# Performance work log

Hardware: AMD Instinct MI355X
Metric: run time of the kernel (lower is better)

Reference implementation:

```python
import jax, jax.numpy as jnp
import numpy as np

BATCH, T, C = 32, 600, 64
DEPTH = 2            # logsig depth 2 -> [increments, Levy areas]
N_SEGMENTS = 50
N_HIDDENS = 512
LOGSIG_CH = C + C * (C - 1) // 2   # 2080, Lyndon-word count at depth 2
IN_SIZE = C + LOGSIG_CH            # 2144 = logsig + start point


def _t_vec(nT, n_segments):
    # matches: [int(round(x)) for x in np.linspace(1, nT, n_segments+1)]
    return np.asarray([int(round(v)) for v in np.linspace(1, nT, n_segments + 1)])


def setup_inputs() -> dict:
    key = jax.random.key(0)
    k0, k1, k2, k3, k4 = jax.random.split(key, 5)
    x = jax.random.normal(k0, (BATCH, T, C), jnp.float32)
    s = 1.0 / np.sqrt(N_HIDDENS)
    w_ih = jax.random.uniform(k1, (4 * N_HIDDENS, IN_SIZE), jnp.float32, -s, s)
    w_hh = jax.random.uniform(k2, (4 * N_HIDDENS, N_HIDDENS), jnp.float32, -s, s)
    b_ih = jax.random.uniform(k3, (4 * N_HIDDENS,), jnp.float32, -s, s)
    b_hh = jax.random.uniform(k4, (4 * N_HIDDENS,), jnp.float32, -s, s)
    return {"x": x, "w_ih": w_ih, "w_hh": w_hh, "b_ih": b_ih, "b_hh": b_hh}


def _logsig_and_start(x):
    """Depth-2 segmented log-signature + segment start points.
    Returns (logsig (B,S,LOGSIG_CH), start (B,S,C))."""
    B, nT, c = x.shape
    tv = _t_vec(nT, N_SEGMENTS)
    starts = tv[:-1] - 1               # segment start frame indices
    ends = tv[1:] - 1                  # segment end frame indices
    # step s (between frames s and s+1) belongs to segment i iff tv[i]-1 <= s < tv[i+1]-1
    step_ids = jnp.asarray(np.searchsorted(tv[1:] - 1, np.arange(nT - 1), side='right'))
    dx = x[:, 1:] - x[:, :-1]                            # (B, T-1, C)
    # per-step outer product x_{t-} (X) dx_t, then segmented sum over steps
    prod = jnp.einsum('btc,btd->btcd', x[:, :-1], dx)    # (B, T-1, C, C)
    Q = jax.ops.segment_sum(jnp.moveaxis(prod, 1, 0), step_ids,
                            num_segments=N_SEGMENTS)      # (S, B, C, C)
    xa = x[:, starts]                                    # (B, S, C)
    xb = x[:, ends]
    inc = xb - xa                                        # level-1 logsig
    # shift origin to segment start: P = sum (X_rel (X) dX)
    P = jnp.moveaxis(Q, 0, 1) - jnp.einsum('bsc,bsd->bscd', xa, inc)
    A = 0.5 * (P - jnp.swapaxes(P, -1, -2))              # Levy area (antisym)
    iu, ju = np.triu_indices(c, 1)                       # Lyndon words (i,j), i<j, lex order
    logsig = jnp.concatenate([inc, A[:, :, iu, ju]], axis=-1)
    return logsig, xa


def _lstm(feats, w_ih, w_hh, b_ih, b_hh):
    B = feats.shape[0]
    H = N_HIDDENS
    gx = jnp.einsum('bsf,gf->bsg', feats, w_ih) + b_ih + b_hh  # (B,S,4H)

    def step(carry, g_t):
        h, cc = carry
        g = g_t + h @ w_hh.T
        i, f, gg, o = jnp.split(g, 4, axis=-1)
        i = jax.nn.sigmoid(i); f = jax.nn.sigmoid(f)
        gg = jnp.tanh(gg); o = jax.nn.sigmoid(o)
        cc = f * cc + i * gg
        h = o * jnp.tanh(cc)
        return (h, cc), h

    h0 = jnp.zeros((B, H), feats.dtype)
    (_, _), hs = jax.lax.scan(step, (h0, h0), jnp.moveaxis(gx, 1, 0))
    return jnp.moveaxis(hs, 0, 1)                        # (B, S, H)


def reference(x, w_ih, w_hh, b_ih, b_hh):
    logsig, x_sp = _logsig_and_start(x)
    feats = jnp.concatenate([logsig, x_sp], axis=-1)      # (B, S, IN_SIZE)
    return _lstm(feats, w_ih, w_hh, b_ih, b_hh)
```

## Files before the change

### kernel.cpp

```cpp
#include <hip/hip_runtime.h>
#include <math.h>

typedef _Float16 f16;
typedef _Float16 f16x8 __attribute__((ext_vector_type(8)));
typedef _Float16 f16x4 __attribute__((ext_vector_type(4)));
typedef float    f32x4 __attribute__((ext_vector_type(4)));

#define BATCH 32
#define TT    600
#define CC    64
#define SEG   50
#define HH    512
#define G4    2048
#define FF    2144
#define MM    1600
#define MP    1664
#define NPAIR 2016
#define CVB   512
#define WRK   208
#define SLOT16 16384

struct TV { int v[51]; };

__device__ __forceinline__ void async_copy16(char* lds, const char* g) {
  __builtin_amdgcn_global_load_lds(
      (const __attribute__((address_space(1))) unsigned int*)g,
      (__attribute__((address_space(3))) unsigned int*)lds, 16, 0, 0);
}

__device__ __forceinline__ float sigm(float x) { return 1.f / (1.f + __expf(-x)); }
__device__ __forceinline__ float tanh_(float x) {
  float ax = fabsf(x);
  float e  = __expf(2.f * ax);
  float t  = 1.f - 2.f / (e + 1.f);
  return x < 0.f ? -t : t;
}
__device__ __forceinline__ unsigned int f16_bits(f16 v) {
  union { f16 f; unsigned short u; } c; c.f = v; return (unsigned int)c.u;
}
__device__ __forceinline__ unsigned int f32_bits(float v) {
  union { float f; unsigned int u; } c; c.f = v; return c.u;
}

__global__ void prep_kernel(const float* __restrict__ x, f16* __restrict__ fhi, TV tv,
                            const float4* __restrict__ w_ih, const float4* __restrict__ w_hh,
                            f16x4* __restrict__ w16, f16x4* __restrict__ whh16,
                            unsigned int* __restrict__ ready) {
  __shared__ float xs[13 * CC];
  int m   = blockIdx.x;
  int tid = threadIdx.x;

  if (m >= MP) {
    int cb   = m - MP;
    int gtid = cb * 256 + tid;
    int nth  = CVB * 256;
    for (int i = gtid; i < G4 * FF / 4; i += nth) {
      float4 v = w_ih[i];
      f16x4 o = {(f16)v.x, (f16)v.y, (f16)v.z, (f16)v.w};
      w16[i] = o;
    }
    for (int i = gtid; i < G4 * HH / 4; i += nth) {
      float4 v = w_hh[i];
      f16x4 o = {(f16)v.x, (f16)v.y, (f16)v.z, (f16)v.w};
      whh16[i] = o;
    }
    if (cb == 0)
      for (int i = tid; i < 544; i += 256) ready[i] = 0u;
    return;
  }

  f16* rhi = fhi + (size_t)m * FF;
  if (m >= MM) {
    unsigned int* a = (unsigned int*)rhi;
    for (int i = tid; i < FF / 2; i += 256) a[i] = 0u;
    return;
  }
  int bb = m & 31, ss = m >> 5;
  int t0 = tv.v[ss] - 1, t1 = tv.v[ss + 1] - 1;
  int len = t1 - t0;
  for (int i = tid; i < (len + 1) * CC; i += 256)
    xs[i] = x[(size_t)bb * TT * CC + (size_t)(t0 + (i >> 6)) * CC + (i & 63)];
  __syncthreads();

  if (tid < CC) {
    float xa  = xs[tid];
    float inc = xs[len * CC + tid] - xa;
    rhi[tid] = (f16)inc;
    rhi[2080 + tid] = (f16)xa;
  }

  int p0 = tid * 8;
  if (p0 < NPAIR) {
    int c = 0, rem = p0;
    while (rem >= 63 - c) { rem -= 63 - c; c++; }
    int d = c + 1 + rem;
    int cs[8], dd[8];
#pragma unroll
    for (int i = 0; i < 8; i++) {
      cs[i] = c; dd[i] = d;
      d++; if (d == 64) { c++; d = c + 1; }
    }
    float acc[8], xc[8], xd[8];
#pragma unroll
    for (int i = 0; i < 8; i++) { acc[i] = 0.f; xc[i] = xs[cs[i]]; xd[i] = xs[dd[i]]; }
    for (int t = 1; t <= len; t++) {
#pragma unroll
      for (int i = 0; i < 8; i++) {
        float nc = xs[t * CC + cs[i]], nd = xs[t * CC + dd[i]];
        acc[i] += xc[i] * (nd - xd[i]) - xd[i] * (nc - xc[i]);
        xc[i] = nc; xd[i] = nd;
      }
    }
#pragma unroll
    for (int i = 0; i < 8; i++) {
      int ci = cs[i], di = dd[i];
      float xac = xs[ci], xad = xs[di];
      float incc = xs[len * CC + ci] - xac, incd = xs[len * CC + di] - xad;
      float v = 0.5f * acc[i] - 0.5f * (xac * incd - xad * incc);
      rhi[64 + p0 + i] = (f16)v;
    }
  }
}

__global__ __launch_bounds__(256) void fused_kernel(
    const f16* __restrict__ fhi, const f16* __restrict__ w16,
    const float* __restrict__ bih, const float* __restrict__ bhh,
    const f16* __restrict__ whh16, float* __restrict__ gx,
    unsigned short* __restrict__ hbuf, unsigned int* __restrict__ ready,
    unsigned int* __restrict__ gxcnt, float* __restrict__ out) {
  __shared__ __align__(16) char smem[40960];
  int tid  = threadIdx.x;
  int lane = tid & 63;

  if (blockIdx.x >= 32) {
    int w  = blockIdx.x - 32;
    int wn = tid >> 6;
    char* ldsA = smem;
    char* ldsB = smem + 4096;
    int rowq = tid >> 2;
    int colq = (tid & 3) * 8;
    int ldst = tid * 16;
    int quad16 = (lane >> 4) * 16;
    int am = lane & 15;
    unsigned int* gxa = (unsigned int*)gx;

    for (int t = 0; t < 2; t++) {
      int id = w + t * WRK;
      int mt = id >> 4, nt = id & 15;
      int m0 = mt * 64, n0 = nt * 128;

      const f16* pa  = fhi + (size_t)(m0 + rowq) * FF + colq;
      const f16* pb0 = w16 + (size_t)(n0 + rowq) * FF + colq;
      const f16* pb1 = pb0 + (size_t)64 * FF;

      f32x4 zero4 = {0.f, 0.f, 0.f, 0.f};
      f32x4 acc[4][2];
#pragma unroll
      for (int i = 0; i < 4; i++) { acc[i][0] = zero4; acc[i][1] = zero4; }

      for (int kt = 0; kt < FF / 32; kt++) {
        int koff = kt * 32;
        async_copy16(ldsA + ldst,        (const char*)(pa + koff));
        async_copy16(ldsB + ldst,        (const char*)(pb0 + koff));
        async_copy16(ldsB + 4096 + ldst, (const char*)(pb1 + koff));
        __syncthreads();

        f16x8 bfr[2];
#pragma unroll
        for (int ni = 0; ni < 2; ni++)
          bfr[ni] = *(const f16x8*)(ldsB + (wn * 32 + ni * 16 + am) * 64 + quad16);
#pragma unroll
        for (int mi = 0; mi < 4; mi++) {
          f16x8 ah = *(const f16x8*)(ldsA + (mi * 16 + am) * 64 + quad16);
#pragma unroll
          for (int ni = 0; ni < 2; ni++)
            acc[mi][ni] = __builtin_amdgcn_mfma_f32_16x16x32_f16(ah, bfr[ni], acc[mi][ni], 0, 0, 0);
        }
        __syncthreads();
      }

#pragma unroll
      for (int ni = 0; ni < 2; ni++) {
        int ncol = n0 + wn * 32 + ni * 16 + (lane & 15);
        float bv = bih[ncol] + bhh[ncol];
#pragma unroll
        for (int mi = 0; mi < 4; mi++) {
          int mrow = m0 + mi * 16 + (lane >> 4) * 4;
#pragma unroll
          for (int r = 0; r < 4; r++)
            __hip_atomic_store(gxa + (size_t)(mrow + r) * G4 + ncol,
                               f32_bits(acc[mi][ni][r] + bv),
                               __ATOMIC_RELAXED, __HIP_MEMORY_SCOPE_AGENT);
        }
      }
      __syncthreads();
      if (tid == 0)
        __hip_atomic_fetch_add(&gxcnt[mt], 1u, __ATOMIC_RELAXED,
                               __HIP_MEMORY_SCOPE_AGENT);
    }
    return;
  }

  f16* hs = (f16*)smem;
  float* gb = (float*)(smem + 32768);

  int gate = tid >> 6;
  int u0   = blockIdx.x * 16;
  int wg   = blockIdx.x;

  f16x8 bf[16];
  {
    const f16* wrow = whh16 + (size_t)(gate * HH + u0 + (lane & 15)) * HH + (lane >> 4) * 8;
#pragma unroll
    for (int ks = 0; ks < 16; ks++) bf[ks] = *(const f16x8*)(wrow + ks * 32);
  }

  int aq  = (lane >> 4);
  int am  = (lane & 15);
  int col = lane & 15;
  int rbase = (lane >> 4) * 4;
  int ub = tid >> 3;
  int uj = tid & 7;
  int koct = (u0 >> 3) + (uj >> 2);
  float cstA = 0.f, cstB = 0.f;

  float gxA[2][4], gxB[2][4];

  for (int s = 0; s < SEG; s++) {
    if (!(s & 1)) {
      if (tid == 0) {
        while (__hip_atomic_load(&gxcnt[s >> 1], __ATOMIC_RELAXED,
                                 __HIP_MEMORY_SCOPE_AGENT) < 16u)
          __builtin_amdgcn_s_sleep(1);
      }
      __syncthreads();
#pragma unroll
      for (int h = 0; h < 2; h++)
#pragma unroll
        for (int r = 0; r < 4; r++) {
          int b = rbase + r;
          gxA[h][r] = gx[(size_t)(((s + h) << 5) + b) * G4 + gate * HH + u0 + col];
          gxB[h][r] = gx[(size_t)(((s + h) << 5) + b + 16) * G4 + gate * HH + u0 + col];
        }
    }

    f32x4 acc0 = {0.f, 0.f, 0.f, 0.f};
    f32x4 acc1 = {0.f, 0.f, 0.f, 0.f};

    if (s > 0) {
      unsigned int tgt = (unsigned int)s;
      if (tid < 32) {
        while (__hip_atomic_load(&ready[tid * 16], __ATOMIC_RELAXED,
                                 __HIP_MEMORY_SCOPE_AGENT) < tgt)
          __builtin_amdgcn_s_sleep(1);
      }
      __syncthreads();

      const char* hrd = (const char*)(hbuf + (size_t)s * SLOT16);
#pragma unroll
      for (int c = 0; c < 8; c++)
        async_copy16((char*)hs + c * 4096 + tid * 16, hrd + c * 4096 + tid * 16);
      __syncthreads();

#pragma unroll
      for (int ks = 0; ks < 16; ks++) {
        f16x8 a0 = *(const f16x8*)((char*)hs + (((ks * 4 + aq) * 32) + am) * 16);
        f16x8 a1 = *(const f16x8*)((char*)hs + (((ks * 4 + aq) * 32) + 16 + am) * 16);
        acc0 = __builtin_amdgcn_mfma_f32_16x16x32_f16(a0, bf[ks], acc0, 0, 0, 0);
        acc1 = __builtin_amdgcn_mfma_f32_16x16x32_f16(a1, bf[ks], acc1, 0, 0, 0);
      }
    }

    int hsel = s & 1;
#pragma unroll
    for (int r = 0; r < 4; r++) {
      int b = rbase + r;
      gb[(gate * 32 + b) * 16 + col]      = acc0[r] + gxA[hsel][r];
      gb[(gate * 32 + b + 16) * 16 + col] = acc1[r] + gxB[hsel][r];
    }
    __syncthreads();

    float2 gi = *(float2*)&gb[(0 * 32 + ub) * 16 + 2 * uj];
    float2 gf = *(float2*)&gb[(1 * 32 + ub) * 16 + 2 * uj];
    float2 gg = *(float2*)&gb[(2 * 32 + ub) * 16 + 2 * uj];
    float2 go = *(float2*)&gb[(3 * 32 + ub) * 16 + 2 * uj];
    cstA = sigm(gf.x) * cstA + sigm(gi.x) * tanh_(gg.x);
    float hA = sigm(go.x) * tanh_(cstA);
    cstB = sigm(gf.y) * cstB + sigm(gi.y) * tanh_(gg.y);
    float hB = sigm(go.y) * tanh_(cstB);

    if (s < SEG - 1) {
      unsigned int hp = f16_bits((f16)hA) | (f16_bits((f16)hB) << 16);
      unsigned int* hwr = (unsigned int*)hbuf + (size_t)(s + 1) * (SLOT16 / 2);
      __hip_atomic_store(hwr + (koct * 32 + ub) * 4 + (uj & 3), hp,
                         __ATOMIC_RELAXED, __HIP_MEMORY_SCOPE_AGENT);
      __syncthreads();
      if (tid == 0)
        __hip_atomic_store(&ready[wg * 16], (unsigned int)(s + 1),
                           __ATOMIC_RELAXED, __HIP_MEMORY_SCOPE_AGENT);
    }
    float2 ho = {hA, hB};
    *(float2*)(out + (size_t)(ub * SEG + s) * HH + u0 + 2 * uj) = ho;
  }
}

extern "C" void kernel_launch(void* const* d_in, const int* in_sizes, int n_in,
                              void* d_out, int out_size, void* d_ws, size_t ws_size,
                              hipStream_t stream) {
  const float* x    = (const float*)d_in[0];
  const float* w_ih = (const float*)d_in[1];
  const float* w_hh = (const float*)d_in[2];
  const float* b_ih = (const float*)d_in[3];
  const float* b_hh = (const float*)d_in[4];
  float* out = (float*)d_out;

  char* ws = (char*)d_ws;
  f16*   fhi   = (f16*)(ws + 0);
  f16*   w16   = (f16*)(ws + 7135232);
  f16*   whh16 = (f16*)(ws + 15921152);
  float* gx    = (float*)(ws + 18018304);
  unsigned short* hbuf  = (unsigned short*)(ws + 31649792);
  unsigned int*   ready = (unsigned int*)(ws + 33288192);

  TV tv;
  double step = 599.0 / 50.0;
  for (int i = 0; i <= 50; i++) {
    double v = (double)i * step + 1.0;
    tv.v[i] = (int)nearbyint(v);
  }
  tv.v[50] = 600;

  unsigned int* gxcnt = ready + 512;

  prep_kernel<<<dim3(MP + CVB), dim3(256), 0, stream>>>(
      x, fhi, tv, (const float4*)w_ih, (const float4*)w_hh,
      (f16x4*)w16, (f16x4*)whh16, ready);

  fused_kernel<<<dim3(32 + WRK), dim3(256), 0, stream>>>(
      fhi, w16, b_ih, b_hh, whh16, gx, hbuf, ready, gxcnt, out);
}
```

Baseline: 270.1 us.

## Remap recurrent MFMA columns so each wave owns whole units, drop block barriers

The recurrent W_hh columns are remapped so each wave computes all four gates for four hidden units. The gate activations can then be combined in a per-wave scratch area with only a waitcnt instead of a block-wide __syncthreads. The ready-flag publish now uses an LDS counter: the last of the four waves to finish signals the step, which removes the remaining barrier. Gate-input loads are now issued every step instead of two steps at a time. The change relies on wave-level LDS visibility and vmcnt ordering being enough to publish h correctly across blocks.

```diff
diff --git a/kernel.cpp b/kernel.cpp
--- a/kernel.cpp
+++ b/kernel.cpp
@@ -128,7 +128,7 @@
     const f16* __restrict__ whh16, float* __restrict__ gx,
     unsigned short* __restrict__ hbuf, unsigned int* __restrict__ ready,
     unsigned int* __restrict__ gxcnt, float* __restrict__ out) {
-  __shared__ __align__(16) char smem[40960];
+  __shared__ __align__(16) char smem[43264];
   int tid  = threadIdx.x;
   int lane = tid & 63;
 
@@ -202,29 +202,33 @@
   }
 
   f16* hs = (f16*)smem;
-  float* gb = (float*)(smem + 32768);
-
-  int gate = tid >> 6;
+  float* scr = (float*)(smem + 32768);
+  unsigned int* cnt = (unsigned int*)(smem + 43008);
+
+  int wave = tid >> 6;
   int u0   = blockIdx.x * 16;
   int wg   = blockIdx.x;
 
+  if (tid < SEG) cnt[tid] = 0u;
+  __syncthreads();
+
   f16x8 bf[16];
   {
-    const f16* wrow = whh16 + (size_t)(gate * HH + u0 + (lane & 15)) * HH + (lane >> 4) * 8;
+    int n = lane & 15;
+    const f16* wrow = whh16 +
+        (size_t)((n & 3) * HH + u0 + wave * 4 + (n >> 2)) * HH + (lane >> 4) * 8;
 #pragma unroll
     for (int ks = 0; ks < 16; ks++) bf[ks] = *(const f16x8*)(wrow + ks * 32);
   }
 
-  int aq  = (lane >> 4);
-  int am  = (lane & 15);
-  int col = lane & 15;
-  int rbase = (lane >> 4) * 4;
-  int ub = tid >> 3;
-  int uj = tid & 7;
-  int koct = (u0 >> 3) + (uj >> 2);
+  int aq = lane >> 4;
+  int am = lane & 15;
+  int gcol = (am & 3) * HH + u0 + wave * 4 + (am >> 2);
+  int ub = lane & 31;
+  int jp = lane >> 5;
+  int ku = u0 + wave * 4 + 2 * jp;
+  float* scw = scr + wave * 640;
   float cstA = 0.f, cstB = 0.f;
-
-  float gxA[2][4], gxB[2][4];
 
   for (int s = 0; s < SEG; s++) {
     if (!(s & 1)) {
@@ -234,14 +238,14 @@
           __builtin_amdgcn_s_sleep(1);
       }
       __syncthreads();
-#pragma unroll
-      for (int h = 0; h < 2; h++)
-#pragma unroll
-        for (int r = 0; r < 4; r++) {
-          int b = rbase + r;
-          gxA[h][r] = gx[(size_t)(((s + h) << 5) + b) * G4 + gate * HH + u0 + col];
-          gxB[h][r] = gx[(size_t)(((s + h) << 5) + b + 16) * G4 + gate * HH + u0 + col];
-        }
+    }
+
+    float gxr0[4], gxr1[4];
+#pragma unroll
+    for (int r = 0; r < 4; r++) {
+      int b = aq * 4 + r;
+      gxr0[r] = gx[(size_t)((s << 5) + b) * G4 + gcol];
+      gxr1[r] = gx[(size_t)((s << 5) + b + 16) * G4 + gcol];
     }
 
     f32x4 acc0 = {0.f, 0.f, 0.f, 0.f};
@@ -271,36 +275,36 @@
       }
     }
 
-    int hsel = s & 1;
 #pragma unroll
     for (int r = 0; r < 4; r++) {
-      int b = rbase + r;
-      gb[(gate * 32 + b) * 16 + col]      = acc0[r] + gxA[hsel][r];
-      gb[(gate * 32 + b + 16) * 16 + col] = acc1[r] + gxB[hsel][r];
-    }
-    __syncthreads();
-
-    float2 gi = *(float2*)&gb[(0 * 32 + ub) * 16 + 2 * uj];
-    float2 gf = *(float2*)&gb[(1 * 32 + ub) * 16 + 2 * uj];
-    float2 gg = *(float2*)&gb[(2 * 32 + ub) * 16 + 2 * uj];
-    float2 go = *(float2*)&gb[(3 * 32 + ub) * 16 + 2 * uj];
-    cstA = sigm(gf.x) * cstA + sigm(gi.x) * tanh_(gg.x);
-    float hA = sigm(go.x) * tanh_(cstA);
-    cstB = sigm(gf.y) * cstB + sigm(gi.y) * tanh_(gg.y);
-    float hB = sigm(go.y) * tanh_(cstB);
+      scw[(aq * 4 + r) * 20 + am]      = acc0[r] + gxr0[r];
+      scw[(16 + aq * 4 + r) * 20 + am] = acc1[r] + gxr1[r];
+    }
+    __asm__ volatile("s_waitcnt lgkmcnt(0)" ::: "memory");
+
+    float4 ga = *(float4*)&scw[ub * 20 + 8 * jp];
+    float4 gb4 = *(float4*)&scw[ub * 20 + 8 * jp + 4];
+    cstA = sigm(ga.y) * cstA + sigm(ga.x) * tanh_(ga.z);
+    float hA = sigm(ga.w) * tanh_(cstA);
+    cstB = sigm(gb4.y) * cstB + sigm(gb4.x) * tanh_(gb4.z);
+    float hB = sigm(gb4.w) * tanh_(cstB);
+
+    float2 ho = {hA, hB};
+    *(float2*)(out + (size_t)(ub * SEG + s) * HH + ku) = ho;
 
     if (s < SEG - 1) {
       unsigned int hp = f16_bits((f16)hA) | (f16_bits((f16)hB) << 16);
       unsigned int* hwr = (unsigned int*)hbuf + (size_t)(s + 1) * (SLOT16 / 2);
-      __hip_atomic_store(hwr + (koct * 32 + ub) * 4 + (uj & 3), hp,
+      __hip_atomic_store(hwr + ((ku >> 3) * 32 + ub) * 4 + ((ku & 7) >> 1), hp,
                          __ATOMIC_RELAXED, __HIP_MEMORY_SCOPE_AGENT);
-      __syncthreads();
-      if (tid == 0)
-        __hip_atomic_store(&ready[wg * 16], (unsigned int)(s + 1),
-                           __ATOMIC_RELAXED, __HIP_MEMORY_SCOPE_AGENT);
-    }
-    float2 ho = {hA, hB};
-    *(float2*)(out + (size_t)(ub * SEG + s) * HH + u0 + 2 * uj) = ho;
+      __asm__ volatile("s_waitcnt vmcnt(0)" ::: "memory");
+      if (lane == 0) {
+        unsigned int old = atomicAdd(&cnt[s], 1u);
+        if (old == 3u)
+          __hip_atomic_store(&ready[wg * 16], (unsigned int)(s + 1),
+                             __ATOMIC_RELAXED, __HIP_MEMORY_SCOPE_AGENT);
+      }
+    }
   }
 }
 
```

New measurement: 284.3 us. 1.05x slower.
